# Kernel optimization log

Measured on AMD Instinct MI355X. Metric: run time of the kernel, lower is better.

Reference implementation:

```python
import jax, jax.numpy as jnp
import numpy as np

B, S, H, A = 2, 512, 128, 7
EPS = 1e-5


def _ln(x, g, b):
    m = jnp.mean(x, axis=-1, keepdims=True)
    v = jnp.var(x, axis=-1, keepdims=True)
    return (x - m) * jax.lax.rsqrt(v + EPS) * g + b


def _gelu(x):
    # repo's custom GeLU is the tanh approximation
    return jax.nn.gelu(x, approximate=True)


def setup_inputs() -> dict:
    key = jax.random.key(0)
    ks = jax.random.split(key, 8)
    w = lambda k, shape: jax.random.normal(k, shape, dtype=jnp.float32) * 0.02
    z = lambda n: jnp.zeros((n,), dtype=jnp.float32)
    o = lambda n: jnp.ones((n,), dtype=jnp.float32)
    return {
        "hiddens": jax.random.normal(ks[0], (B, S, H), dtype=jnp.float32),
        # action head: Linear(H,H) -> GeLU -> LN(H) -> Linear(H,A) -> LogSoftmax(dim=1)
        "aw1": w(ks[1], (H, H)), "ab1": z(H),
        "a_ln_g": o(H), "a_ln_b": z(H),
        "aw2": w(ks[2], (H, A)), "ab2": z(A),
        # left pointer head
        "lhid_w": w(ks[3], (H, H)), "lhid_b": z(H),
        "lhead_w": w(ks[4], (H, H)), "lhead_b": z(H),
        "l_ln_g": o(H), "l_ln_b": z(H),
        "l_proj_w": w(ks[5], (H, 1)), "l_proj_b": z(1),
        # right pointer head
        "rhid_w": w(ks[6], (H, H)), "rhid_b": z(H),
        "rhead_w": w(ks[7], (H, H)), "rhead_b": z(H),
        "r_ln_g": o(H), "r_ln_b": z(H),
        "r_proj_w": w(jax.random.fold_in(key, 99), (H, 1)), "r_proj_b": z(1),
    }


def reference(hiddens, aw1, ab1, a_ln_g, a_ln_b, aw2, ab2,
              lhid_w, lhid_b, lhead_w, lhead_b, l_ln_g, l_ln_b, l_proj_w, l_proj_b,
              rhid_w, rhid_b, rhead_w, rhead_b, r_ln_g, r_ln_b, r_proj_w, r_proj_b):
    # action head; note: original applies LogSoftmax over dim=1 (sequence dim)
    act_h = _ln(_gelu(hiddens @ aw1 + ab1), a_ln_g, a_ln_b)  # [B,S,H]
    actions = jax.nn.log_softmax(act_h @ aw2 + ab2, axis=1)   # [B,S,A]

    def ptr(hid_w, hid_b, head_w, head_b, ln_g, ln_b, pw, pb):
        hv = hiddens @ hid_w + hid_b    # [B,S,H] ("hiddens" branch -> broadcast over dim 1)
        hd = hiddens @ head_w + head_b  # [B,S,H] ("heads" branch   -> broadcast over dim 2)
        pair = hv[:, None, :, :] + hd[:, :, None, :]            # [B,S,S,H]
        scores = (_ln(_gelu(pair), ln_g, ln_b) @ pw)[..., 0] + pb[0]  # [B,S,S]
        return jax.nn.log_softmax(scores, axis=2)

    lefts = ptr(lhid_w, lhid_b, lhead_w, lhead_b, l_ln_g, l_ln_b, l_proj_w, l_proj_b)
    rights = ptr(rhid_w, rhid_b, rhead_w, rhead_b, r_ln_g, r_ln_b, r_proj_w, r_proj_b)
    return (actions, lefts, rights)
```

## Files before the change

### kernel.cpp

```cpp
#include <hip/hip_runtime.h>
#include <math.h>

#define EPS 1e-5f

typedef float v2f __attribute__((ext_vector_type(2)));

#define R0 0.39892715f
#define R1 -0.06655040f
#define R2 0.00972280f
#define R3 -0.00095163f
#define R4 0.0000439966f

__device__ __forceinline__ float poly_gelu(float v) {
    float s = v * v;
    s = fminf(s, 6.25f);
    float q = fmaf(R4, s, R3);
    q = fmaf(q, s, R2);
    q = fmaf(q, s, R1);
    q = fmaf(q, s, R0);
    return v * fmaf(v, q, 0.5f);
}

__device__ __forceinline__ void acc2(v2f a, v2f d, v2f gpv, v2f& s1, v2f& s2, v2f& s3) {
    v2f x = a + d;
    v2f s = x * x;
    s = __builtin_elementwise_min(s, (v2f)(6.25f));
    v2f q = __builtin_elementwise_fma(s, (v2f)(R4), (v2f)(R3));
    q = __builtin_elementwise_fma(q, s, (v2f)(R2));
    q = __builtin_elementwise_fma(q, s, (v2f)(R1));
    q = __builtin_elementwise_fma(q, s, (v2f)(R0));
    v2f u = __builtin_elementwise_fma(x, q, (v2f)(0.5f));
    v2f gl = x * u;
    s1 += gl;
    s2 = __builtin_elementwise_fma(gl, gl, s2);
    s3 = __builtin_elementwise_fma(gl, gpv, s3);
}

__device__ __forceinline__ v2f mk2(float a, float b) { v2f r; r.x = a; r.y = b; return r; }

__global__ __launch_bounds__(256) void k_gemm5(
    const float* __restrict__ hiddens,
    const float* __restrict__ w0, const float* __restrict__ b0,
    const float* __restrict__ w1, const float* __restrict__ b1,
    const float* __restrict__ w2, const float* __restrict__ b2,
    const float* __restrict__ w3, const float* __restrict__ b3,
    const float* __restrict__ w4, const float* __restrict__ b4,
    const float* __restrict__ a_ln_g,
    const float* __restrict__ aw2,
    float* __restrict__ logits,
    float* __restrict__ o1, float* __restrict__ o2,
    float* __restrict__ o3, float* __restrict__ o4)
{
    __shared__ float hs[8 * 128];
    __shared__ float sred[4][43];
    const int mat = blockIdx.y;
    const float* W; const float* Bv; float* O;
    switch (mat) {
        case 0: W = w0; Bv = b0; O = o1; break;
        case 1: W = w1; Bv = b1; O = o1; break;
        case 2: W = w2; Bv = b2; O = o2; break;
        case 3: W = w3; Bv = b3; O = o3; break;
        default: W = w4; Bv = b4; O = o4; break;
    }
    const int rowbase = blockIdx.x * 8;
    const int t = threadIdx.x;
    *(float4*)&hs[t * 4] = *(const float4*)&hiddens[rowbase * 128 + t * 4];
    __syncthreads();

    const int n = t & 127, half = t >> 7;
    float acc[4] = {0.f, 0.f, 0.f, 0.f};
    for (int k = 0; k < 128; k += 4) {
        const float wv0 = W[(k + 0) * 128 + n];
        const float wv1 = W[(k + 1) * 128 + n];
        const float wv2 = W[(k + 2) * 128 + n];
        const float wv3 = W[(k + 3) * 128 + n];
        #pragma unroll
        for (int rr = 0; rr < 4; ++rr) {
            const float4 h4 = *(const float4*)&hs[(half * 4 + rr) * 128 + k];
            acc[rr] = fmaf(h4.x, wv0, acc[rr]);
            acc[rr] = fmaf(h4.y, wv1, acc[rr]);
            acc[rr] = fmaf(h4.z, wv2, acc[rr]);
            acc[rr] = fmaf(h4.w, wv3, acc[rr]);
        }
    }
    const float bias = Bv[n];

    if (mat != 0) {
        #pragma unroll
        for (int rr = 0; rr < 4; ++rr)
            O[(rowbase + half * 4 + rr) * 128 + n] = acc[rr] + bias;
        return;
    }

    const float gt = a_ln_g[n];
    float vals[43];
    float gw[7];
    #pragma unroll
    for (int a = 0; a < 7; ++a) {
        gw[a] = gt * aw2[n * 7 + a];
        vals[36 + a] = gw[a];
    }
    #pragma unroll
    for (int rr = 0; rr < 4; ++rr) {
        const float x = poly_gelu(acc[rr] + bias);
        vals[rr] = x;
        vals[4 + rr] = x * x;
        #pragma unroll
        for (int a = 0; a < 7; ++a) vals[8 + rr * 7 + a] = x * gw[a];
    }
    #pragma unroll
    for (int q = 0; q < 43; ++q)
        for (int m = 1; m <= 32; m <<= 1)
            vals[q] += __shfl_xor(vals[q], m, 64);

    const int wave = t >> 6, lane = t & 63;
    if (lane == 0) {
        #pragma unroll
        for (int q = 0; q < 43; ++q) sred[wave][q] = vals[q];
    }
    __syncthreads();

    if (t < 56) {
        const int r8 = t / 7, a = t - r8 * 7;
        const int h2 = r8 >> 2, rr = r8 & 3;
        const float* u0 = sred[h2 * 2];
        const float* u1 = sred[h2 * 2 + 1];
        const float S1 = u0[rr] + u1[rr];
        const float S2 = u0[4 + rr] + u1[4 + rr];
        const float T  = u0[8 + rr * 7 + a] + u1[8 + rr * 7 + a];
        const float Ga = u0[36 + a] + u1[36 + a];
        const float mean = S1 * (1.0f / 128.0f);
        const float var  = fmaf(-mean, mean, S2 * (1.0f / 128.0f));
        const float inv  = __builtin_amdgcn_rsqf(var + EPS);
        const int srow = rowbase + h2 * 4 + rr;
        const int b = srow >> 9, s = srow & 511;
        logits[(b * 7 + a) * 512 + s] = fmaf(inv, fmaf(-mean, Ga, T), 0.0f);
    }
}

__global__ __launch_bounds__(256) void k_fused(
    const float* __restrict__ logits,
    const float* __restrict__ l_hv, const float* __restrict__ l_hd,
    const float* __restrict__ r_hv, const float* __restrict__ r_hd,
    const float* __restrict__ l_g, const float* __restrict__ l_pw,
    const float* __restrict__ r_g, const float* __restrict__ r_pw,
    float* __restrict__ out)
{
    const int gbl = blockIdx.x;
    const int t = threadIdx.x;
    const int lane = t & 63, wave = t >> 6;

    __shared__ float red[8];

    if (gbl < 14) {
        const int b = gbl / 7, a = gbl % 7;
        const float v0 = logits[(b * 7 + a) * 512 + t];
        const float v1 = logits[(b * 7 + a) * 512 + t + 256];
        float m = fmaxf(v0, v1);
        for (int mm = 1; mm <= 32; mm <<= 1) m = fmaxf(m, __shfl_xor(m, mm, 64));
        if (lane == 0) red[wave] = m;
        __syncthreads();
        m = fmaxf(fmaxf(red[0], red[1]), fmaxf(red[2], red[3]));
        float e = __expf(v0 - m) + __expf(v1 - m);
        for (int mm = 1; mm <= 32; mm <<= 1) e += __shfl_xor(e, mm, 64);
        if (lane == 0) red[4 + wave] = e;
        __syncthreads();
        const float tot = red[4] + red[5] + red[6] + red[7];
        const float L = m + __logf(tot);
        out[b * 3584 + t * 7 + a] = v0 - L;
        out[b * 3584 + (t + 256) * 7 + a] = v1 - L;
        return;
    }

    const int p = gbl - 14;
    const int head = p >> 8;
    const int b = (p >> 7) & 1;
    const int i0 = (p & 127) * 4;

    const float* hv = (head ? r_hv : l_hv) + b * 512 * 128;
    const float* hd = (head ? r_hd : l_hd) + b * 512 * 128;
    const float* g  = head ? r_g  : l_g;
    const float* pw = head ? r_pw : l_pw;
    float* obase = out + (head ? 531456 : 7168) + (b * 512 + i0) * 512;

    __shared__ float hv_s[64 * 132];
    __shared__ float hd_s[4 * 132];
    __shared__ float gp_s[128];
    __shared__ float sc_s[4 * 512];
    __shared__ float redc[2];

    if (t < 128) {
        float gv = g[t] * pw[t];
        gp_s[t] = gv;
        for (int mm = 1; mm <= 32; mm <<= 1) gv += __shfl_xor(gv, mm, 64);
        if ((t & 63) == 0) redc[t >> 6] = gv;
    }
    if (t < 128) {
        const int row = t >> 5, c = t & 31;
        *(float4*)&hd_s[row * 132 + c * 4] = *(const float4*)(hd + (i0 + row) * 128 + c * 4);
    }
    __syncthreads();
    const float G = redc[0] + redc[1];

    const int i = wave;
    const int j = lane;
    const float* D = hd_s + i * 132;

    for (int c = 0; c < 8; ++c) {
        const int j0 = c * 64;
        #pragma unroll
        for (int k = 0; k < 8; ++k) {
            const int idx = k * 256 + t;
            const int row = idx >> 5, col = idx & 31;
            *(float4*)&hv_s[row * 132 + col * 4] =
                *(const float4*)(hv + (j0 + row) * 128 + col * 4);
        }
        __syncthreads();

        const float* A = hv_s + j * 132;
        v2f s1 = (v2f)(0.f), s2 = (v2f)(0.f), s3 = (v2f)(0.f);
        #pragma unroll 4
        for (int h = 0; h < 128; h += 4) {
            const float4 a4 = *(const float4*)(A + h);
            const float4 d4 = *(const float4*)(D + h);
            const float4 g4 = *(const float4*)(gp_s + h);
            acc2(mk2(a4.x, a4.y), mk2(d4.x, d4.y), mk2(g4.x, g4.y), s1, s2, s3);
            acc2(mk2(a4.z, a4.w), mk2(d4.z, d4.w), mk2(g4.z, g4.w), s1, s2, s3);
        }
        const float S1 = s1.x + s1.y, S2 = s2.x + s2.y, S3 = s3.x + s3.y;
        const float mean = S1 * (1.0f / 128.0f);
        const float var  = fmaf(-mean, mean, S2 * (1.0f / 128.0f));
        const float inv  = __builtin_amdgcn_rsqf(var + EPS);
        sc_s[i * 512 + j0 + j] = fmaf(inv, fmaf(-mean, G, S3), 0.0f);
        __syncthreads();
    }

    float v[8];
    {
        const float4 p0 = *(const float4*)&sc_s[i * 512 + lane * 8];
        const float4 p1 = *(const float4*)&sc_s[i * 512 + lane * 8 + 4];
        v[0] = p0.x; v[1] = p0.y; v[2] = p0.z; v[3] = p0.w;
        v[4] = p1.x; v[5] = p1.y; v[6] = p1.z; v[7] = p1.w;
    }
    float m = v[0];
    #pragma unroll
    for (int k = 1; k < 8; ++k) m = fmaxf(m, v[k]);
    for (int mm = 1; mm <= 32; mm <<= 1) m = fmaxf(m, __shfl_xor(m, mm, 64));
    float e = 0.f;
    #pragma unroll
    for (int k = 0; k < 8; ++k) e += __expf(v[k] - m);
    for (int mm = 1; mm <= 32; mm <<= 1) e += __shfl_xor(e, mm, 64);
    const float L = m + __logf(e);

    float* orow = obase + i * 512;
    float4 w0, w1;
    w0.x = v[0] - L; w0.y = v[1] - L; w0.z = v[2] - L; w0.w = v[3] - L;
    w1.x = v[4] - L; w1.y = v[5] - L; w1.z = v[6] - L; w1.w = v[7] - L;
    *(float4*)&orow[lane * 8] = w0;
    *(float4*)&orow[lane * 8 + 4] = w1;
}

extern "C" void kernel_launch(void* const* d_in, const int* in_sizes, int n_in,
                              void* d_out, int out_size, void* d_ws, size_t ws_size,
                              hipStream_t stream)
{
    const float* hiddens  = (const float*)d_in[0];
    const float* aw1      = (const float*)d_in[1];
    const float* ab1      = (const float*)d_in[2];
    const float* a_ln_g   = (const float*)d_in[3];
    const float* aw2      = (const float*)d_in[5];
    const float* lhid_w   = (const float*)d_in[7];
    const float* lhid_b   = (const float*)d_in[8];
    const float* lhead_w  = (const float*)d_in[9];
    const float* lhead_b  = (const float*)d_in[10];
    const float* l_ln_g   = (const float*)d_in[11];
    const float* l_proj_w = (const float*)d_in[13];
    const float* rhid_w   = (const float*)d_in[15];
    const float* rhid_b   = (const float*)d_in[16];
    const float* rhead_w  = (const float*)d_in[17];
    const float* rhead_b  = (const float*)d_in[18];
    const float* r_ln_g   = (const float*)d_in[19];
    const float* r_proj_w = (const float*)d_in[21];

    float* ws      = (float*)d_ws;
    float* l_hv    = ws;
    float* l_hd    = ws + 131072;
    float* r_hv    = ws + 262144;
    float* r_hd    = ws + 393216;
    float* logits  = ws + 524288;
    float* out     = (float*)d_out;

    k_gemm5<<<dim3(128, 5), 256, 0, stream>>>(
        hiddens, aw1, ab1, lhid_w, lhid_b, lhead_w, lhead_b,
        rhid_w, rhid_b, rhead_w, rhead_b,
        a_ln_g, aw2, logits,
        l_hv, l_hd, r_hv, r_hd);
    k_fused<<<526, 256, 0, stream>>>(
        logits, l_hv, l_hd, r_hv, r_hd,
        l_ln_g, l_proj_w, r_ln_g, r_proj_w, out);
}
```

Before: 146.9 us.

## Compute pairwise GeLU-LN scores in packed fp16 with 2D tiling and separate log-softmax

Stores the hidden projections as fp16 and evaluates the pairwise GeLU polynomial in packed half2 math, accumulating the LayerNorm sums with fdot2 into fp32. The fused per-row kernel is replaced by a 32x32 tiled pair-score kernel in which each thread computes a 2x2 block, reusing operands held in registers. A separate kernel then does the row log-softmax in place on the output. This targets ALU throughput and shared-memory traffic, at the cost of fp16 precision in the GeLU and an extra global round trip of the score matrix.

```diff
diff --git a/kernel.cpp b/kernel.cpp
--- a/kernel.cpp
+++ b/kernel.cpp
@@ -3,7 +3,7 @@
 
 #define EPS 1e-5f
 
-typedef float v2f __attribute__((ext_vector_type(2)));
+typedef _Float16 h2 __attribute__((ext_vector_type(2)));
 
 #define R0 0.39892715f
 #define R1 -0.06655040f
@@ -21,22 +21,34 @@
     return v * fmaf(v, q, 0.5f);
 }
 
-__device__ __forceinline__ void acc2(v2f a, v2f d, v2f gpv, v2f& s1, v2f& s2, v2f& s3) {
-    v2f x = a + d;
-    v2f s = x * x;
-    s = __builtin_elementwise_min(s, (v2f)(6.25f));
-    v2f q = __builtin_elementwise_fma(s, (v2f)(R4), (v2f)(R3));
-    q = __builtin_elementwise_fma(q, s, (v2f)(R2));
-    q = __builtin_elementwise_fma(q, s, (v2f)(R1));
-    q = __builtin_elementwise_fma(q, s, (v2f)(R0));
-    v2f u = __builtin_elementwise_fma(x, q, (v2f)(0.5f));
-    v2f gl = x * u;
-    s1 += gl;
-    s2 = __builtin_elementwise_fma(gl, gl, s2);
-    s3 = __builtin_elementwise_fma(gl, gpv, s3);
-}
-
-__device__ __forceinline__ v2f mk2(float a, float b) { v2f r; r.x = a; r.y = b; return r; }
+#define HC0 0.3989425f
+#define HC1 -0.0662041f
+#define HC2 0.00908457f
+#define HC3 -0.000637973f
+
+#if __has_builtin(__builtin_amdgcn_fdot2)
+#define DOT2(a, b, c) __builtin_amdgcn_fdot2((a), (b), (c), false)
+#else
+#define DOT2(a, b, c) fmaf((float)(a).x, (float)(b).x, fmaf((float)(a).y, (float)(b).y, (c)))
+#endif
+
+__device__ __forceinline__ h2 bc_h2(unsigned v) { return __builtin_bit_cast(h2, v); }
+
+__device__ __forceinline__ void acc2h(h2 a, h2 d, h2 gp,
+                                      float& s1, float& s2, float& s3) {
+    const h2 ones = (h2)(_Float16)1.0f;
+    h2 x = a + d;
+    h2 s = x * x;
+    s = __builtin_elementwise_min(s, (h2)(_Float16)6.25f);
+    h2 q = __builtin_elementwise_fma(s, (h2)(_Float16)HC3, (h2)(_Float16)HC2);
+    q = __builtin_elementwise_fma(q, s, (h2)(_Float16)HC1);
+    q = __builtin_elementwise_fma(q, s, (h2)(_Float16)HC0);
+    h2 u = __builtin_elementwise_fma(x, q, (h2)(_Float16)0.5f);
+    h2 gl = x * u;
+    s1 = DOT2(gl, ones, s1);
+    s2 = DOT2(gl, gl, s2);
+    s3 = DOT2(gl, gp, s3);
+}
 
 __global__ __launch_bounds__(256) void k_gemm5(
     const float* __restrict__ hiddens,
@@ -48,13 +60,13 @@
     const float* __restrict__ a_ln_g,
     const float* __restrict__ aw2,
     float* __restrict__ logits,
-    float* __restrict__ o1, float* __restrict__ o2,
-    float* __restrict__ o3, float* __restrict__ o4)
+    _Float16* __restrict__ o1, _Float16* __restrict__ o2,
+    _Float16* __restrict__ o3, _Float16* __restrict__ o4)
 {
     __shared__ float hs[8 * 128];
     __shared__ float sred[4][43];
     const int mat = blockIdx.y;
-    const float* W; const float* Bv; float* O;
+    const float* W; const float* Bv; _Float16* O;
     switch (mat) {
         case 0: W = w0; Bv = b0; O = o1; break;
         case 1: W = w1; Bv = b1; O = o1; break;
@@ -88,7 +100,7 @@
     if (mat != 0) {
         #pragma unroll
         for (int rr = 0; rr < 4; ++rr)
-            O[(rowbase + half * 4 + rr) * 128 + n] = acc[rr] + bias;
+            O[(rowbase + half * 4 + rr) * 128 + n] = (_Float16)(acc[rr] + bias);
         return;
     }
 
@@ -122,9 +134,9 @@
 
     if (t < 56) {
         const int r8 = t / 7, a = t - r8 * 7;
-        const int h2 = r8 >> 2, rr = r8 & 3;
-        const float* u0 = sred[h2 * 2];
-        const float* u1 = sred[h2 * 2 + 1];
+        const int h2i = r8 >> 2, rr = r8 & 3;
+        const float* u0 = sred[h2i * 2];
+        const float* u1 = sred[h2i * 2 + 1];
         const float S1 = u0[rr] + u1[rr];
         const float S2 = u0[4 + rr] + u1[4 + rr];
         const float T  = u0[8 + rr * 7 + a] + u1[8 + rr * 7 + a];
@@ -132,28 +144,107 @@
         const float mean = S1 * (1.0f / 128.0f);
         const float var  = fmaf(-mean, mean, S2 * (1.0f / 128.0f));
         const float inv  = __builtin_amdgcn_rsqf(var + EPS);
-        const int srow = rowbase + h2 * 4 + rr;
+        const int srow = rowbase + h2i * 4 + rr;
         const int b = srow >> 9, s = srow & 511;
-        logits[(b * 7 + a) * 512 + s] = fmaf(inv, fmaf(-mean, Ga, T), 0.0f);
-    }
-}
-
-__global__ __launch_bounds__(256) void k_fused(
-    const float* __restrict__ logits,
-    const float* __restrict__ l_hv, const float* __restrict__ l_hd,
-    const float* __restrict__ r_hv, const float* __restrict__ r_hd,
+        logits[(b * 7 + a) * 512 + s] = inv * fmaf(-mean, Ga, T);
+    }
+}
+
+__global__ __launch_bounds__(256) void k_pair_scores(
+    const _Float16* __restrict__ l_hv, const _Float16* __restrict__ l_hd,
+    const _Float16* __restrict__ r_hv, const _Float16* __restrict__ r_hd,
     const float* __restrict__ l_g, const float* __restrict__ l_pw,
     const float* __restrict__ r_g, const float* __restrict__ r_pw,
     float* __restrict__ out)
 {
+    const int head = blockIdx.z >> 1, b = blockIdx.z & 1;
+    const int i0 = blockIdx.y * 32, j0 = blockIdx.x * 32;
+
+    const _Float16* hv = (head ? r_hv : l_hv) + b * 512 * 128;
+    const _Float16* hd = (head ? r_hd : l_hd) + b * 512 * 128;
+    const float* g  = head ? r_g  : l_g;
+    const float* pw = head ? r_pw : l_pw;
+    float* o = out + (head ? 531456 : 7168) + (b * 512 + i0) * 512 + j0;
+
+    __shared__ __align__(16) _Float16 hv_s[32 * 136];
+    __shared__ __align__(16) _Float16 hd_s[32 * 136];
+    __shared__ __align__(16) _Float16 gp_s[128];
+    __shared__ float redc[2];
+    const int t = threadIdx.x;
+
+    if (t < 128) {
+        const float gv = g[t] * pw[t];
+        gp_s[t] = (_Float16)gv;
+        float r = gv;
+        for (int mm = 1; mm <= 32; mm <<= 1) r += __shfl_xor(r, mm, 64);
+        if ((t & 63) == 0) redc[t >> 6] = r;
+    }
+
+    #pragma unroll
+    for (int k = 0; k < 2; ++k) {
+        const int slot = k * 256 + t;
+        const int row = slot >> 4, col = slot & 15;
+        *(uint4*)(hv_s + row * 136 + col * 8) =
+            *(const uint4*)(hv + (j0 + row) * 128 + col * 8);
+        *(uint4*)(hd_s + row * 136 + col * 8) =
+            *(const uint4*)(hd + (i0 + row) * 128 + col * 8);
+    }
+    __syncthreads();
+
+    const float G = redc[0] + redc[1];
+
+    const int tj = t & 15, ti = t >> 4;
+    const _Float16* A0 = hv_s + tj * 136;
+    const _Float16* A1 = hv_s + (tj + 16) * 136;
+    const _Float16* D0 = hd_s + (2 * ti) * 136;
+    const _Float16* D1 = hd_s + (2 * ti + 1) * 136;
+
+    float s1[4] = {0.f, 0.f, 0.f, 0.f};
+    float s2[4] = {0.f, 0.f, 0.f, 0.f};
+    float s3[4] = {0.f, 0.f, 0.f, 0.f};
+
+#define PSTEP(c) { \
+    const h2 av0 = bc_h2(a0.c), av1 = bc_h2(a1.c); \
+    const h2 dv0 = bc_h2(d0.c), dv1 = bc_h2(d1.c); \
+    const h2 gv = bc_h2(gp.c); \
+    acc2h(av0, dv0, gv, s1[0], s2[0], s3[0]); \
+    acc2h(av1, dv0, gv, s1[1], s2[1], s3[1]); \
+    acc2h(av0, dv1, gv, s1[2], s2[2], s3[2]); \
+    acc2h(av1, dv1, gv, s1[3], s2[3], s3[3]); }
+
+    #pragma unroll 2
+    for (int h = 0; h < 128; h += 8) {
+        const uint4 a0 = *(const uint4*)(A0 + h);
+        const uint4 a1 = *(const uint4*)(A1 + h);
+        const uint4 d0 = *(const uint4*)(D0 + h);
+        const uint4 d1 = *(const uint4*)(D1 + h);
+        const uint4 gp = *(const uint4*)(gp_s + h);
+        PSTEP(x) PSTEP(y) PSTEP(z) PSTEP(w)
+    }
+#undef PSTEP
+
+    #pragma unroll
+    for (int p = 0; p < 4; ++p) {
+        const float mean = s1[p] * (1.0f / 128.0f);
+        const float var  = fmaf(-mean, mean, s2[p] * (1.0f / 128.0f));
+        const float inv  = __builtin_amdgcn_rsqf(var + EPS);
+        const int ii = 2 * ti + (p >> 1);
+        const int jj = tj + 16 * (p & 1);
+        o[ii * 512 + jj] = inv * fmaf(-mean, G, s3[p]);
+    }
+}
+
+__global__ __launch_bounds__(256) void k_lsm(
+    float* __restrict__ out, const float* __restrict__ logits)
+{
     const int gbl = blockIdx.x;
     const int t = threadIdx.x;
-    const int lane = t & 63, wave = t >> 6;
-
+    const int wave = t >> 6, lane = t & 63;
     __shared__ float red[8];
 
-    if (gbl < 14) {
-        const int b = gbl / 7, a = gbl % 7;
+    if (gbl >= 2048) {
+        const int idx = gbl - 2048;
+        const int b = idx / 7, a = idx % 7;
         const float v0 = logits[(b * 7 + a) * 512 + t];
         const float v1 = logits[(b * 7 + a) * 512 + t + 256];
         float m = fmaxf(v0, v1);
@@ -172,92 +263,21 @@
         return;
     }
 
-    const int p = gbl - 14;
-    const int head = p >> 8;
-    const int b = (p >> 7) & 1;
-    const int i0 = (p & 127) * 4;
-
-    const float* hv = (head ? r_hv : l_hv) + b * 512 * 128;
-    const float* hd = (head ? r_hd : l_hd) + b * 512 * 128;
-    const float* g  = head ? r_g  : l_g;
-    const float* pw = head ? r_pw : l_pw;
-    float* obase = out + (head ? 531456 : 7168) + (b * 512 + i0) * 512;
-
-    __shared__ float hv_s[64 * 132];
-    __shared__ float hd_s[4 * 132];
-    __shared__ float gp_s[128];
-    __shared__ float sc_s[4 * 512];
-    __shared__ float redc[2];
-
-    if (t < 128) {
-        float gv = g[t] * pw[t];
-        gp_s[t] = gv;
-        for (int mm = 1; mm <= 32; mm <<= 1) gv += __shfl_xor(gv, mm, 64);
-        if ((t & 63) == 0) redc[t >> 6] = gv;
-    }
-    if (t < 128) {
-        const int row = t >> 5, c = t & 31;
-        *(float4*)&hd_s[row * 132 + c * 4] = *(const float4*)(hd + (i0 + row) * 128 + c * 4);
-    }
-    __syncthreads();
-    const float G = redc[0] + redc[1];
-
-    const int i = wave;
-    const int j = lane;
-    const float* D = hd_s + i * 132;
-
-    for (int c = 0; c < 8; ++c) {
-        const int j0 = c * 64;
-        #pragma unroll
-        for (int k = 0; k < 8; ++k) {
-            const int idx = k * 256 + t;
-            const int row = idx >> 5, col = idx & 31;
-            *(float4*)&hv_s[row * 132 + col * 4] =
-                *(const float4*)(hv + (j0 + row) * 128 + col * 4);
-        }
-        __syncthreads();
-
-        const float* A = hv_s + j * 132;
-        v2f s1 = (v2f)(0.f), s2 = (v2f)(0.f), s3 = (v2f)(0.f);
-        #pragma unroll 4
-        for (int h = 0; h < 128; h += 4) {
-            const float4 a4 = *(const float4*)(A + h);
-            const float4 d4 = *(const float4*)(D + h);
-            const float4 g4 = *(const float4*)(gp_s + h);
-            acc2(mk2(a4.x, a4.y), mk2(d4.x, d4.y), mk2(g4.x, g4.y), s1, s2, s3);
-            acc2(mk2(a4.z, a4.w), mk2(d4.z, d4.w), mk2(g4.z, g4.w), s1, s2, s3);
-        }
-        const float S1 = s1.x + s1.y, S2 = s2.x + s2.y, S3 = s3.x + s3.y;
-        const float mean = S1 * (1.0f / 128.0f);
-        const float var  = fmaf(-mean, mean, S2 * (1.0f / 128.0f));
-        const float inv  = __builtin_amdgcn_rsqf(var + EPS);
-        sc_s[i * 512 + j0 + j] = fmaf(inv, fmaf(-mean, G, S3), 0.0f);
-        __syncthreads();
-    }
-
-    float v[8];
-    {
-        const float4 p0 = *(const float4*)&sc_s[i * 512 + lane * 8];
-        const float4 p1 = *(const float4*)&sc_s[i * 512 + lane * 8 + 4];
-        v[0] = p0.x; v[1] = p0.y; v[2] = p0.z; v[3] = p0.w;
-        v[4] = p1.x; v[5] = p1.y; v[6] = p1.z; v[7] = p1.w;
-    }
-    float m = v[0];
-    #pragma unroll
-    for (int k = 1; k < 8; ++k) m = fmaxf(m, v[k]);
+    float* p = out + (gbl >= 1024 ? 531456 : 7168) + (gbl & 1023) * 512;
+    const float v0 = p[t], v1 = p[t + 256];
+    float m = fmaxf(v0, v1);
     for (int mm = 1; mm <= 32; mm <<= 1) m = fmaxf(m, __shfl_xor(m, mm, 64));
-    float e = 0.f;
-    #pragma unroll
-    for (int k = 0; k < 8; ++k) e += __expf(v[k] - m);
+    if (lane == 0) red[wave] = m;
+    __syncthreads();
+    m = fmaxf(fmaxf(red[0], red[1]), fmaxf(red[2], red[3]));
+    float e = __expf(v0 - m) + __expf(v1 - m);
     for (int mm = 1; mm <= 32; mm <<= 1) e += __shfl_xor(e, mm, 64);
-    const float L = m + __logf(e);
-
-    float* orow = obase + i * 512;
-    float4 w0, w1;
-    w0.x = v[0] - L; w0.y = v[1] - L; w0.z = v[2] - L; w0.w = v[3] - L;
-    w1.x = v[4] - L; w1.y = v[5] - L; w1.z = v[6] - L; w1.w = v[7] - L;
-    *(float4*)&orow[lane * 8] = w0;
-    *(float4*)&orow[lane * 8 + 4] = w1;
+    if (lane == 0) red[4 + wave] = e;
+    __syncthreads();
+    const float tot = red[4] + red[5] + red[6] + red[7];
+    const float L = m + __logf(tot);
+    p[t] = v0 - L;
+    p[t + 256] = v1 - L;
 }
 
 extern "C" void kernel_launch(void* const* d_in, const int* in_sizes, int n_in,
@@ -282,12 +302,12 @@
     const float* r_ln_g   = (const float*)d_in[19];
     const float* r_proj_w = (const float*)d_in[21];
 
-    float* ws      = (float*)d_ws;
-    float* l_hv    = ws;
-    float* l_hd    = ws + 131072;
-    float* r_hv    = ws + 262144;
-    float* r_hd    = ws + 393216;
-    float* logits  = ws + 524288;
+    _Float16* hws = (_Float16*)d_ws;
+    _Float16* l_hv = hws;
+    _Float16* l_hd = hws + 131072;
+    _Float16* r_hv = hws + 262144;
+    _Float16* r_hd = hws + 393216;
+    float* logits  = (float*)(hws + 524288);
     float* out     = (float*)d_out;
 
     k_gemm5<<<dim3(128, 5), 256, 0, stream>>>(
@@ -295,7 +315,8 @@
         rhid_w, rhid_b, rhead_w, rhead_b,
         a_ln_g, aw2, logits,
         l_hv, l_hd, r_hv, r_hd);
-    k_fused<<<526, 256, 0, stream>>>(
-        logits, l_hv, l_hd, r_hv, r_hd,
+    k_pair_scores<<<dim3(16, 16, 4), 256, 0, stream>>>(
+        l_hv, l_hd, r_hv, r_hd,
         l_ln_g, l_proj_w, r_ln_g, r_proj_w, out);
-}
+    k_lsm<<<2062, 256, 0, stream>>>(out, logits);
+}
```

New measurement: 139.0 us. 1.06x faster.
